# Performance work log

Hardware: AMD Instinct MI355X
Metric: run time of the kernel (lower is better)

The kernel has to match this reference:

```python
import jax, jax.numpy as jnp
import numpy as np

BETA = 0.25
N_CODES = 1024
CODE_DIM = 64


def setup_inputs() -> dict:
    key = jax.random.key(0)
    k1, k2 = jax.random.split(key)
    z_e = jax.random.normal(k1, (32, CODE_DIM, 2048), dtype=jnp.float32)
    # nn.init.uniform_(weight, -1/n_codes, 1/n_codes)
    lim = 1.0 / N_CODES
    codebook = jax.random.uniform(k2, (N_CODES, CODE_DIM), dtype=jnp.float32,
                                  minval=-lim, maxval=lim)
    return {"z_e": z_e, "codebook": codebook}


def reference(z_e, codebook):
    B, C, K = z_e.shape
    # (B, C, K) -> (B*K, C)
    z = jnp.transpose(z_e, (0, 2, 1)).reshape(-1, C)
    # squared L2 distances: ||z||^2 + ||e||^2 - 2 z.e  -> (N, n_codes)
    dist = (jnp.sum(z * z, axis=1, keepdims=True)
            + jnp.sum(codebook * codebook, axis=1)[None, :]
            - 2.0 * (z @ codebook.T))
    codes = jnp.argmin(dist, axis=1)  # (N,)
    # gather quantized vectors, back to (B, C, K)
    z_q = jnp.transpose(codebook[codes].reshape(B, K, C), (0, 2, 1))
    # straight-through
    z_q_st = z_e + jax.lax.stop_gradient(z_q - z_e)
    sg = jax.lax.stop_gradient
    loss_codebook = jnp.mean((z_q - sg(z_e)) ** 2)
    loss_commit = jnp.mean((z_e - sg(z_q)) ** 2)
    loss_vq = loss_codebook + BETA * loss_commit
    # perplexity via histogram (equivalent to onehot.mean(0))
    n = codes.shape[0]
    avg_probs = jnp.zeros((N_CODES,), dtype=jnp.float32).at[codes].add(1.0) / n
    perplexity = jnp.exp(-jnp.sum(avg_probs * jnp.log(avg_probs + 1e-10)))
    return z_q_st, codes.reshape(B, K), loss_vq, perplexity
```

## Files before the change

### kernel.cpp

```cpp
#include <hip/hip_runtime.h>
#include <math.h>

#define NB 32
#define NC 64
#define NK 2048
#define NCODES 1024
#define NVEC (NB*NK)
#define NELEM (NB*NC*NK)
#define NBLK (NVEC/64)

#define MARGIN 1.5e-3f
#define CAP 32

#define WS_HIST  0
#define WS_CBN32 4096
#define WS_PART  8192
#define WS_CBBF  32768

typedef __bf16 bf16x8 __attribute__((ext_vector_type(8)));
typedef float  f32x4  __attribute__((ext_vector_type(4)));
#define MFMA16(A, B, ACC) __builtin_amdgcn_mfma_f32_16x16x32_bf16(A, B, ACC, 0, 0, 0)

__global__ void k_cbprep(const float* __restrict__ cb, float* __restrict__ n32,
                         __bf16* __restrict__ cbbf, int* __restrict__ hist) {
    const int t = threadIdx.x;
    const int j = blockIdx.x * 64 + t;
    if (blockIdx.x == 0) {
        int4 z4; z4.x = 0; z4.y = 0; z4.z = 0; z4.w = 0;
#pragma unroll
        for (int i = 0; i < 4; i++) ((int4*)hist)[t * 4 + i] = z4;
    }
    const float* cr = cb + (size_t)j * NC;
    float x[64];
#pragma unroll
    for (int i = 0; i < 16; i++) {
        f32x4 tv = *(const f32x4*)(cr + 4 * i);
        x[4*i+0] = tv[0]; x[4*i+1] = tv[1]; x[4*i+2] = tv[2]; x[4*i+3] = tv[3];
    }
    float r[8];
#pragma unroll
    for (int q = 0; q < 8; q++) r[q] = __fmul_rn(x[q], x[q]);
#pragma unroll
    for (int i = 8; i < 64; i += 8)
#pragma unroll
        for (int q = 0; q < 8; q++)
            r[q] = __fadd_rn(r[q], __fmul_rn(x[i + q], x[i + q]));
    float s01 = __fadd_rn(r[0], r[1]), s23 = __fadd_rn(r[2], r[3]);
    float s45 = __fadd_rn(r[4], r[5]), s67 = __fadd_rn(r[6], r[7]);
    n32[j] = __fadd_rn(__fadd_rn(s01, s23), __fadd_rn(s45, s67));
    __bf16* br = cbbf + (size_t)j * NC;
#pragma unroll
    for (int i = 0; i < 8; i++) {
        bf16x8 o;
#pragma unroll
        for (int q = 0; q < 8; q++) o[q] = (__bf16)x[8*i + q];
        *(bf16x8*)(br + 8*i) = o;
    }
}

__launch_bounds__(256, 4)
__global__ void k_vq(const float* __restrict__ ze, const float* __restrict__ cb,
                     const float* __restrict__ n32, const __bf16* __restrict__ cbbf,
                     int* __restrict__ hist, float* __restrict__ codes_f,
                     float* __restrict__ outq, double* __restrict__ part) {
    __shared__ float wmin[64][4];
    __shared__ float gthr[64];
    __shared__ int cnt[64];
    __shared__ int cand[64][CAP];
    __shared__ unsigned long long keys2[64][4];
    __shared__ int codearr[64];
    __shared__ double lsd[4];

    const int t = threadIdx.x;
    const int L = t & 63;
    const int w = t >> 6;
    const int quad = L >> 4;
    const int col = L & 15;
    const int vec0 = blockIdx.x * 64;
    const int b = vec0 >> 11;
    const int k0 = vec0 & (NK - 1);
    const float* zbase = ze + (size_t)b * NC * NK + k0;

    bf16x8 af[4][2];
#pragma unroll
    for (int vt = 0; vt < 4; vt++)
#pragma unroll
        for (int kt = 0; kt < 2; kt++)
#pragma unroll
            for (int j = 0; j < 8; j++)
                af[vt][kt][j] =
                    (__bf16)zbase[(size_t)(kt*32 + quad*8 + j) * NK + vt*16 + col];

    float pmin[4][4];
#pragma unroll
    for (int vt = 0; vt < 4; vt++)
#pragma unroll
        for (int r = 0; r < 4; r++) pmin[vt][r] = 1e30f;
#pragma unroll 4
    for (int tile = 0; tile < 16; tile++) {
        const __bf16* brow = cbbf + (size_t)(w*256 + tile*16 + col) * NC + quad*8;
        bf16x8 b0 = *(const bf16x8*)(brow);
        bf16x8 b1 = *(const bf16x8*)(brow + 32);
        float nvv = n32[w*256 + tile*16 + col];
#pragma unroll
        for (int vt = 0; vt < 4; vt++) {
            f32x4 acc = {0.f, 0.f, 0.f, 0.f};
            acc = MFMA16(af[vt][0], b0, acc);
            acc = MFMA16(af[vt][1], b1, acc);
#pragma unroll
            for (int r = 0; r < 4; r++) {
                float pd = __fsub_rn(nvv, __fmul_rn(2.f, acc[r]));
                pmin[vt][r] = fminf(pmin[vt][r], pd);
            }
        }
    }
#pragma unroll
    for (int vt = 0; vt < 4; vt++)
#pragma unroll
        for (int r = 0; r < 4; r++) {
            float pm = pmin[vt][r];
            pm = fminf(pm, __shfl_xor(pm, 1, 16));
            pm = fminf(pm, __shfl_xor(pm, 2, 16));
            pm = fminf(pm, __shfl_xor(pm, 4, 16));
            pm = fminf(pm, __shfl_xor(pm, 8, 16));
            if (col == 0) wmin[vt*16 + quad*4 + r][w] = pm;
        }
    __syncthreads();

    if (t < 64) {
        float g = wmin[t][0];
#pragma unroll
        for (int ww = 1; ww < 4; ww++) g = fminf(g, wmin[t][ww]);
        gthr[t] = g + MARGIN;
        cnt[t] = 0;
    }
    __syncthreads();

    float thr[4][4];
#pragma unroll
    for (int vt = 0; vt < 4; vt++)
#pragma unroll
        for (int r = 0; r < 4; r++) thr[vt][r] = gthr[vt*16 + quad*4 + r];
#pragma unroll 4
    for (int tile = 0; tile < 16; tile++) {
        const __bf16* brow = cbbf + (size_t)(w*256 + tile*16 + col) * NC + quad*8;
        bf16x8 b0 = *(const bf16x8*)(brow);
        bf16x8 b1 = *(const bf16x8*)(brow + 32);
        float nvv = n32[w*256 + tile*16 + col];
#pragma unroll
        for (int vt = 0; vt < 4; vt++) {
            f32x4 acc = {0.f, 0.f, 0.f, 0.f};
            acc = MFMA16(af[vt][0], b0, acc);
            acc = MFMA16(af[vt][1], b1, acc);
#pragma unroll
            for (int r = 0; r < 4; r++) {
                float pd = __fsub_rn(nvv, __fmul_rn(2.f, acc[r]));
                if (pd <= thr[vt][r]) {
                    int m = vt*16 + quad*4 + r;
                    int slot = atomicAdd(&cnt[m], 1);
                    if (slot < CAP) cand[m][slot] = w*256 + tile*16 + col;
                }
            }
        }
    }
    __syncthreads();

    {
        const int v = L;
        float rr[8];
#pragma unroll
        for (int q = 0; q < 8; q++) {
            float xx = zbase[(size_t)q * NK + v];
            rr[q] = __fmul_rn(xx, xx);
        }
#pragma unroll
        for (int i = 8; i < 64; i += 8)
#pragma unroll
            for (int q = 0; q < 8; q++) {
                float xx = zbase[(size_t)(i + q) * NK + v];
                rr[q] = __fadd_rn(rr[q], __fmul_rn(xx, xx));
            }
        float s01 = __fadd_rn(rr[0], rr[1]), s23 = __fadd_rn(rr[2], rr[3]);
        float s45 = __fadd_rn(rr[4], rr[5]), s67 = __fadd_rn(rr[6], rr[7]);
        float t1 = __fadd_rn(__fadd_rn(s01, s23), __fadd_rn(s45, s67));

        int cc = cnt[v];
        unsigned long long kmin = 0xFFFFFFFFFFFFFFFFULL;
        if (cc <= CAP) {
            for (int si = w; si < cc; si += 4) {
                int j = cand[v][si];
                const float* cr = cb + (size_t)j * NC;
                float a = 0.f;
#pragma unroll
                for (int c = 0; c < NC; c++)
                    a = __fmaf_rn(zbase[(size_t)c * NK + v], cr[c], a);
                float d = __fsub_rn(__fadd_rn(t1, n32[j]), __fmul_rn(2.f, a));
                unsigned long long key =
                    ((unsigned long long)__float_as_uint(d) << 32) | (unsigned int)j;
                if (key < kmin) kmin = key;
            }
        } else {
            for (int j = w * 256; j < (w + 1) * 256; j++) {
                const float* cr = cb + (size_t)j * NC;
                float a = 0.f;
#pragma unroll
                for (int c = 0; c < NC; c++)
                    a = __fmaf_rn(zbase[(size_t)c * NK + v], cr[c], a);
                float d = __fsub_rn(__fadd_rn(t1, n32[j]), __fmul_rn(2.f, a));
                unsigned long long key =
                    ((unsigned long long)__float_as_uint(d) << 32) | (unsigned int)j;
                if (key < kmin) kmin = key;
            }
        }
        keys2[v][w] = kmin;
    }
    __syncthreads();

    if (t < 64) {
        unsigned long long kmin = keys2[t][0];
#pragma unroll
        for (int ww = 1; ww < 4; ww++) {
            unsigned long long kk = keys2[t][ww];
            if (kk < kmin) kmin = kk;
        }
        int code = (int)(kmin & 0xFFFFFFFFu);
        codearr[t] = code;
        codes_f[vec0 + t] = (float)code;
        atomicAdd(&hist[code], 1);
    }
    __syncthreads();

    double s = 0.0;
    float* ob = outq + (size_t)b * NC * NK + k0;
    const int c0 = t >> 4;
    const int v0 = (t & 15) * 4;
    int cds[4];
#pragma unroll
    for (int u = 0; u < 4; u++) cds[u] = codearr[v0 + u];
#pragma unroll
    for (int half = 0; half < 4; half++) {
        const int c = c0 + half * 16;
        f32x4 zv = *(const f32x4*)(zbase + (size_t)c * NK + v0);
        f32x4 ov;
#pragma unroll
        for (int u = 0; u < 4; u++) {
            float qv = cb[(size_t)cds[u] * NC + c];
            ov[u] = __fadd_rn(zv[u], __fsub_rn(qv, zv[u]));
            double d = (double)qv - (double)zv[u];
            s += d * d;
        }
        *(f32x4*)(ob + (size_t)c * NK + v0) = ov;
    }
    for (int off = 32; off; off >>= 1) s += __shfl_down(s, off);
    if (L == 0) lsd[w] = s;
    __syncthreads();
    if (t == 0) {
        double tot = 0.0;
#pragma unroll
        for (int i = 0; i < 4; i++) tot += lsd[i];
        part[blockIdx.x] = tot;
    }
}

__launch_bounds__(1024)
__global__ void k_final(const double* __restrict__ part, const int* __restrict__ hist,
                        float* __restrict__ out) {
    int t = threadIdx.x;
    double vL = part[t];
    double p = (double)hist[t] * (1.0 / (double)NVEC);
    double vE = p * log(p + 1e-10);
    for (int off = 32; off; off >>= 1) {
        vL += __shfl_down(vL, off);
        vE += __shfl_down(vE, off);
    }
    __shared__ double lsL[16], lsE[16];
    int lane = t & 63, wv = t >> 6;
    if (lane == 0) { lsL[wv] = vL; lsE[wv] = vE; }
    __syncthreads();
    if (t == 0) {
        double SL = 0.0, SE = 0.0;
        for (int i = 0; i < 16; i++) { SL += lsL[i]; SE += lsE[i]; }
        double loss_cb = SL / (double)NELEM;
        out[NELEM + NVEC]     = (float)(loss_cb + 0.25 * loss_cb);
        out[NELEM + NVEC + 1] = (float)exp(-SE);
    }
}

extern "C" void kernel_launch(void* const* d_in, const int* in_sizes, int n_in,
                              void* d_out, int out_size, void* d_ws, size_t ws_size,
                              hipStream_t stream) {
    const float* ze = (const float*)d_in[0];
    const float* cb = (const float*)d_in[1];
    float* out = (float*)d_out;
    char* ws = (char*)d_ws;

    int*    hist = (int*)(ws + WS_HIST);
    float*  n32  = (float*)(ws + WS_CBN32);
    double* part = (double*)(ws + WS_PART);
    __bf16* cbbf = (__bf16*)(ws + WS_CBBF);

    float* zq      = out;
    float* codes_f = out + NELEM;

    k_cbprep<<<16, 64, 0, stream>>>(cb, n32, cbbf, hist);
    k_vq<<<NBLK, 256, 0, stream>>>(ze, cb, n32, cbbf, hist, codes_f, zq, part);
    k_final<<<1, 1024, 0, stream>>>(part, hist, out);
}
```

Baseline: 128.4 us.

## Stage z tile and code norms in LDS; fuse final reduction via last-block counter

Loads each block's 64x64 z tile (padded) and the codebook norms into shared memory once, and serves the bf16 fragment build, norm computation, candidate rescoring and output pass from LDS instead of repeated strided global loads. Removes the separate finalization kernel by having the last block (detected with an atomic counter reset in the prep kernel) compute the loss and perplexity. The change costs more LDS per block, which could limit occupancy, plus an extra sync and a threadfence.

```diff
diff --git a/kernel.cpp b/kernel.cpp
--- a/kernel.cpp
+++ b/kernel.cpp
@@ -15,6 +15,7 @@
 #define WS_HIST  0
 #define WS_CBN32 4096
 #define WS_PART  8192
+#define WS_CTR   16384
 #define WS_CBBF  32768
 
 typedef __bf16 bf16x8 __attribute__((ext_vector_type(8)));
@@ -22,13 +23,15 @@
 #define MFMA16(A, B, ACC) __builtin_amdgcn_mfma_f32_16x16x32_bf16(A, B, ACC, 0, 0, 0)
 
 __global__ void k_cbprep(const float* __restrict__ cb, float* __restrict__ n32,
-                         __bf16* __restrict__ cbbf, int* __restrict__ hist) {
+                         __bf16* __restrict__ cbbf, int* __restrict__ hist,
+                         unsigned int* __restrict__ ctr) {
     const int t = threadIdx.x;
     const int j = blockIdx.x * 64 + t;
     if (blockIdx.x == 0) {
         int4 z4; z4.x = 0; z4.y = 0; z4.z = 0; z4.w = 0;
 #pragma unroll
         for (int i = 0; i < 4; i++) ((int4*)hist)[t * 4 + i] = z4;
+        if (t == 0) *ctr = 0u;
     }
     const float* cr = cb + (size_t)j * NC;
     float x[64];
@@ -62,7 +65,10 @@
 __global__ void k_vq(const float* __restrict__ ze, const float* __restrict__ cb,
                      const float* __restrict__ n32, const __bf16* __restrict__ cbbf,
                      int* __restrict__ hist, float* __restrict__ codes_f,
-                     float* __restrict__ outq, double* __restrict__ part) {
+                     float* __restrict__ outq, double* __restrict__ part,
+                     unsigned int* __restrict__ ctr, float* __restrict__ outsc) {
+    __shared__ float zl[64 * 65];
+    __shared__ float nl[NCODES];
     __shared__ float wmin[64][4];
     __shared__ float gthr[64];
     __shared__ int cnt[64];
@@ -70,6 +76,8 @@
     __shared__ unsigned long long keys2[64][4];
     __shared__ int codearr[64];
     __shared__ double lsd[4];
+    __shared__ int lastflag;
+    __shared__ double TL[16], TE[16];
 
     const int t = threadIdx.x;
     const int L = t & 63;
@@ -81,6 +89,19 @@
     const int k0 = vec0 & (NK - 1);
     const float* zbase = ze + (size_t)b * NC * NK + k0;
 
+#pragma unroll
+    for (int i = 0; i < 4; i++) {
+        int idx = t + i * 256;
+        int c = idx >> 4, vq = (idx & 15) * 4;
+        f32x4 val = *(const f32x4*)(zbase + (size_t)c * NK + vq);
+        zl[c * 65 + vq + 0] = val[0];
+        zl[c * 65 + vq + 1] = val[1];
+        zl[c * 65 + vq + 2] = val[2];
+        zl[c * 65 + vq + 3] = val[3];
+        nl[idx] = n32[idx];
+    }
+    __syncthreads();
+
     bf16x8 af[4][2];
 #pragma unroll
     for (int vt = 0; vt < 4; vt++)
@@ -89,7 +110,7 @@
 #pragma unroll
             for (int j = 0; j < 8; j++)
                 af[vt][kt][j] =
-                    (__bf16)zbase[(size_t)(kt*32 + quad*8 + j) * NK + vt*16 + col];
+                    (__bf16)zl[(kt*32 + quad*8 + j) * 65 + vt*16 + col];
 
     float pmin[4][4];
 #pragma unroll
@@ -101,7 +122,7 @@
         const __bf16* brow = cbbf + (size_t)(w*256 + tile*16 + col) * NC + quad*8;
         bf16x8 b0 = *(const bf16x8*)(brow);
         bf16x8 b1 = *(const bf16x8*)(brow + 32);
-        float nvv = n32[w*256 + tile*16 + col];
+        float nvv = nl[w*256 + tile*16 + col];
 #pragma unroll
         for (int vt = 0; vt < 4; vt++) {
             f32x4 acc = {0.f, 0.f, 0.f, 0.f};
@@ -146,7 +167,7 @@
         const __bf16* brow = cbbf + (size_t)(w*256 + tile*16 + col) * NC + quad*8;
         bf16x8 b0 = *(const bf16x8*)(brow);
         bf16x8 b1 = *(const bf16x8*)(brow + 32);
-        float nvv = n32[w*256 + tile*16 + col];
+        float nvv = nl[w*256 + tile*16 + col];
 #pragma unroll
         for (int vt = 0; vt < 4; vt++) {
             f32x4 acc = {0.f, 0.f, 0.f, 0.f};
@@ -170,14 +191,14 @@
         float rr[8];
 #pragma unroll
         for (int q = 0; q < 8; q++) {
-            float xx = zbase[(size_t)q * NK + v];
+            float xx = zl[q * 65 + v];
             rr[q] = __fmul_rn(xx, xx);
         }
 #pragma unroll
         for (int i = 8; i < 64; i += 8)
 #pragma unroll
             for (int q = 0; q < 8; q++) {
-                float xx = zbase[(size_t)(i + q) * NK + v];
+                float xx = zl[(i + q) * 65 + v];
                 rr[q] = __fadd_rn(rr[q], __fmul_rn(xx, xx));
             }
         float s01 = __fadd_rn(rr[0], rr[1]), s23 = __fadd_rn(rr[2], rr[3]);
@@ -193,8 +214,8 @@
                 float a = 0.f;
 #pragma unroll
                 for (int c = 0; c < NC; c++)
-                    a = __fmaf_rn(zbase[(size_t)c * NK + v], cr[c], a);
-                float d = __fsub_rn(__fadd_rn(t1, n32[j]), __fmul_rn(2.f, a));
+                    a = __fmaf_rn(zl[c * 65 + v], cr[c], a);
+                float d = __fsub_rn(__fadd_rn(t1, nl[j]), __fmul_rn(2.f, a));
                 unsigned long long key =
                     ((unsigned long long)__float_as_uint(d) << 32) | (unsigned int)j;
                 if (key < kmin) kmin = key;
@@ -205,8 +226,8 @@
                 float a = 0.f;
 #pragma unroll
                 for (int c = 0; c < NC; c++)
-                    a = __fmaf_rn(zbase[(size_t)c * NK + v], cr[c], a);
-                float d = __fsub_rn(__fadd_rn(t1, n32[j]), __fmul_rn(2.f, a));
+                    a = __fmaf_rn(zl[c * 65 + v], cr[c], a);
+                float d = __fsub_rn(__fadd_rn(t1, nl[j]), __fmul_rn(2.f, a));
                 unsigned long long key =
                     ((unsigned long long)__float_as_uint(d) << 32) | (unsigned int)j;
                 if (key < kmin) kmin = key;
@@ -240,13 +261,13 @@
 #pragma unroll
     for (int half = 0; half < 4; half++) {
         const int c = c0 + half * 16;
-        f32x4 zv = *(const f32x4*)(zbase + (size_t)c * NK + v0);
         f32x4 ov;
 #pragma unroll
         for (int u = 0; u < 4; u++) {
+            float zev = zl[c * 65 + v0 + u];
             float qv = cb[(size_t)cds[u] * NC + c];
-            ov[u] = __fadd_rn(zv[u], __fsub_rn(qv, zv[u]));
-            double d = (double)qv - (double)zv[u];
+            ov[u] = __fadd_rn(zev, __fsub_rn(qv, zev));
+            double d = (double)qv - (double)zev;
             s += d * d;
         }
         *(f32x4*)(ob + (size_t)c * NK + v0) = ov;
@@ -255,34 +276,37 @@
     if (L == 0) lsd[w] = s;
     __syncthreads();
     if (t == 0) {
-        double tot = 0.0;
-#pragma unroll
-        for (int i = 0; i < 4; i++) tot += lsd[i];
+        double tot = lsd[0] + lsd[1] + lsd[2] + lsd[3];
         part[blockIdx.x] = tot;
-    }
-}
-
-__launch_bounds__(1024)
-__global__ void k_final(const double* __restrict__ part, const int* __restrict__ hist,
-                        float* __restrict__ out) {
-    int t = threadIdx.x;
-    double vL = part[t];
-    double p = (double)hist[t] * (1.0 / (double)NVEC);
-    double vE = p * log(p + 1e-10);
-    for (int off = 32; off; off >>= 1) {
-        vL += __shfl_down(vL, off);
-        vE += __shfl_down(vE, off);
-    }
-    __shared__ double lsL[16], lsE[16];
-    int lane = t & 63, wv = t >> 6;
-    if (lane == 0) { lsL[wv] = vL; lsE[wv] = vE; }
-    __syncthreads();
-    if (t == 0) {
-        double SL = 0.0, SE = 0.0;
-        for (int i = 0; i < 16; i++) { SL += lsL[i]; SE += lsE[i]; }
-        double loss_cb = SL / (double)NELEM;
-        out[NELEM + NVEC]     = (float)(loss_cb + 0.25 * loss_cb);
-        out[NELEM + NVEC + 1] = (float)exp(-SE);
+        __threadfence();
+        unsigned int my = atomicAdd(ctr, 1u);
+        lastflag = (my == NBLK - 1) ? 1 : 0;
+    }
+    __syncthreads();
+
+    if (lastflag) {
+        __threadfence();
+#pragma unroll
+        for (int gi = 0; gi < 4; gi++) {
+            int g = w + gi * 4;
+            double vL = part[g * 64 + L];
+            double p = (double)hist[g * 64 + L] * (1.0 / (double)NVEC);
+            double vE = p * log(p + 1e-10);
+            for (int off = 32; off; off >>= 1) {
+                vL += __shfl_down(vL, off);
+                vE += __shfl_down(vE, off);
+            }
+            if (L == 0) { TL[g] = vL; TE[g] = vE; }
+        }
+        __syncthreads();
+        if (t == 0) {
+            double SL = 0.0, SE = 0.0;
+#pragma unroll
+            for (int i = 0; i < 16; i++) { SL += TL[i]; SE += TE[i]; }
+            double loss_cb = SL / (double)NELEM;
+            outsc[0] = (float)(loss_cb + 0.25 * loss_cb);
+            outsc[1] = (float)exp(-SE);
+        }
     }
 }
 
@@ -294,15 +318,17 @@
     float* out = (float*)d_out;
     char* ws = (char*)d_ws;
 
-    int*    hist = (int*)(ws + WS_HIST);
-    float*  n32  = (float*)(ws + WS_CBN32);
-    double* part = (double*)(ws + WS_PART);
-    __bf16* cbbf = (__bf16*)(ws + WS_CBBF);
+    int*          hist = (int*)(ws + WS_HIST);
+    float*        n32  = (float*)(ws + WS_CBN32);
+    double*       part = (double*)(ws + WS_PART);
+    unsigned int* ctr  = (unsigned int*)(ws + WS_CTR);
+    __bf16*       cbbf = (__bf16*)(ws + WS_CBBF);
 
     float* zq      = out;
     float* codes_f = out + NELEM;
-
-    k_cbprep<<<16, 64, 0, stream>>>(cb, n32, cbbf, hist);
-    k_vq<<<NBLK, 256, 0, stream>>>(ze, cb, n32, cbbf, hist, codes_f, zq, part);
-    k_final<<<1, 1024, 0, stream>>>(part, hist, out);
+    float* outsc   = out + NELEM + NVEC;
+
+    k_cbprep<<<16, 64, 0, stream>>>(cb, n32, cbbf, hist, ctr);
+    k_vq<<<NBLK, 256, 0, stream>>>(ze, cb, n32, cbbf, hist, codes_f, zq, part,
+                                   ctr, outsc);
 }
```

After: 151.9 us. 1.18x slower.
